# Performance work log

Hardware: AMD Instinct MI355X
Metric: run time of the kernel (lower is better)

## Reference

```python
import jax, jax.numpy as jnp
import numpy as np

H = 256
L = 5
B = 1024
NL, EL = 65536, 262144
NP_, EP = 131072, 524288
BN_EPS = 1e-5


def _bn_relu(x, gamma, beta):
    # BatchNorm1d (training mode, biased variance) followed by ReLU
    m = x.mean(axis=0)
    v = ((x - m) ** 2).mean(axis=0)
    return jax.nn.relu((x - m) * jax.lax.rsqrt(v + BN_EPS) * gamma + beta)


def _gin_conv(h, src, dst, W1, b1, W2, b2):
    # GINConv, eps=0: mlp(x + sum_{j->i} x_j)
    agg = jax.ops.segment_sum(h[src], dst, num_segments=h.shape[0])
    z = h + agg
    return jax.nn.relu(z @ W1 + b1) @ W2 + b2


def _forward(lig_x, prot_x, lig_embed_W, lig_embed_b, prot_embed_W, prot_embed_b,
             lig_virtual0, prot_virtual0,
             lig_conv_W1, lig_conv_b1, lig_conv_W2, lig_conv_b2,
             lig_vmlp_W, lig_vmlp_b, lig_vmlp_gamma, lig_vmlp_beta,
             prot_conv_W1, prot_conv_b1, prot_conv_W2, prot_conv_b2,
             prot_vmlp_W, prot_vmlp_b, prot_vmlp_gamma, prot_vmlp_beta,
             pred_W1, pred_b1, pred_W2, pred_b2,
             lig_batch, prot_batch, lig_edge_index, prot_edge_index):
    lig_h = lig_x @ lig_embed_W + lig_embed_b        # [NL, H]
    prot_h = prot_x @ prot_embed_W + prot_embed_b    # [NP, H]
    lig_v = jnp.broadcast_to(lig_virtual0, (B, H))
    prot_v = jnp.broadcast_to(prot_virtual0, (B, H))
    l_src, l_dst = lig_edge_index[0], lig_edge_index[1]
    p_src, p_dst = prot_edge_index[0], prot_edge_index[1]
    for i in range(L):
        # ligand branch: virtual-node pool -> MLP -> broadcast, then GIN conv (residual)
        lig_v = lig_v + jax.ops.segment_sum(lig_h, lig_batch, num_segments=B)
        lig_v = _bn_relu(lig_v @ lig_vmlp_W[i] + lig_vmlp_b[i], lig_vmlp_gamma[i], lig_vmlp_beta[i])
        lig_h = lig_h + lig_v[lig_batch]
        lig_h = lig_h + _gin_conv(lig_h, l_src, l_dst, lig_conv_W1[i], lig_conv_b1[i], lig_conv_W2[i], lig_conv_b2[i])
        # protein branch
        prot_v = prot_v + jax.ops.segment_sum(prot_h, prot_batch, num_segments=B)
        prot_v = _bn_relu(prot_v @ prot_vmlp_W[i] + prot_vmlp_b[i], prot_vmlp_gamma[i], prot_vmlp_beta[i])
        prot_h = prot_h + prot_v[prot_batch]
        prot_h = prot_h + _gin_conv(prot_h, p_src, p_dst, prot_conv_W1[i], prot_conv_b1[i], prot_conv_W2[i], prot_conv_b2[i])
    lig_cnt = jax.ops.segment_sum(jnp.ones((lig_h.shape[0],), lig_h.dtype), lig_batch, num_segments=B)
    prot_cnt = jax.ops.segment_sum(jnp.ones((prot_h.shape[0],), prot_h.dtype), prot_batch, num_segments=B)
    lig_pool = jax.ops.segment_sum(lig_h, lig_batch, num_segments=B) / lig_cnt[:, None]
    prot_pool = jax.ops.segment_sum(prot_h, prot_batch, num_segments=B) / prot_cnt[:, None]
    combined = jnp.concatenate([lig_pool, prot_pool], axis=-1)  # [B, 2H]
    return jax.nn.relu(combined @ pred_W1 + pred_b1) @ pred_W2 + pred_b2  # [B, 1]


def setup_inputs() -> dict:
    key = jax.random.key(0)
    ks = jax.random.split(key, 40)
    s = 0.05
    inp = {
        'lig_x': jax.random.normal(ks[0], (NL, 26), jnp.float32),
        'prot_x': jax.random.normal(ks[1], (NP_, 20), jnp.float32),
        'lig_embed_W': jax.random.normal(ks[2], (26, H), jnp.float32) * s,
        'lig_embed_b': jnp.zeros((H,), jnp.float32),
        'prot_embed_W': jax.random.normal(ks[3], (20, H), jnp.float32) * s,
        'prot_embed_b': jnp.zeros((H,), jnp.float32),
        'lig_virtual0': jax.random.normal(ks[4], (1, H), jnp.float32),
        'prot_virtual0': jax.random.normal(ks[5], (1, H), jnp.float32),
        'lig_conv_W1': jax.random.normal(ks[6], (L, H, H), jnp.float32) * s,
        'lig_conv_b1': jnp.zeros((L, H), jnp.float32),
        'lig_conv_W2': jax.random.normal(ks[7], (L, H, H), jnp.float32) * s,
        'lig_conv_b2': jnp.zeros((L, H), jnp.float32),
        'lig_vmlp_W': jax.random.normal(ks[8], (L, H, H), jnp.float32) * s,
        'lig_vmlp_b': jnp.zeros((L, H), jnp.float32),
        'lig_vmlp_gamma': jnp.ones((L, H), jnp.float32),
        'lig_vmlp_beta': jnp.zeros((L, H), jnp.float32),
        'prot_conv_W1': jax.random.normal(ks[9], (L, H, H), jnp.float32) * s,
        'prot_conv_b1': jnp.zeros((L, H), jnp.float32),
        'prot_conv_W2': jax.random.normal(ks[10], (L, H, H), jnp.float32) * s,
        'prot_conv_b2': jnp.zeros((L, H), jnp.float32),
        'prot_vmlp_W': jax.random.normal(ks[11], (L, H, H), jnp.float32) * s,
        'prot_vmlp_b': jnp.zeros((L, H), jnp.float32),
        'prot_vmlp_gamma': jnp.ones((L, H), jnp.float32),
        'prot_vmlp_beta': jnp.zeros((L, H), jnp.float32),
        'pred_W1': jax.random.normal(ks[12], (2 * H, H), jnp.float32) * s,
        'pred_b1': jnp.zeros((H,), jnp.float32),
        'pred_W2': jax.random.normal(ks[13], (H, 1), jnp.float32) * s,
        'pred_b2': jnp.zeros((1,), jnp.float32),
        # sorted batch ids covering all B graphs (PyG-style contiguous batching)
        'lig_batch': (jnp.arange(NL, dtype=jnp.int32) * B) // NL,
        'prot_batch': (jnp.arange(NP_, dtype=jnp.int32) * B) // NP_,
        'lig_edge_index': jax.random.randint(ks[14], (2, EL), 0, NL, jnp.int32),
        'prot_edge_index': jax.random.randint(ks[15], (2, EP), 0, NP_, jnp.int32),
    }
    return inp


def reference(lig_x, prot_x, lig_embed_W, lig_embed_b, prot_embed_W, prot_embed_b,
              lig_virtual0, prot_virtual0,
              lig_conv_W1, lig_conv_b1, lig_conv_W2, lig_conv_b2,
              lig_vmlp_W, lig_vmlp_b, lig_vmlp_gamma, lig_vmlp_beta,
              prot_conv_W1, prot_conv_b1, prot_conv_W2, prot_conv_b2,
              prot_vmlp_W, prot_vmlp_b, prot_vmlp_gamma, prot_vmlp_beta,
              pred_W1, pred_b1, pred_W2, pred_b2,
              lig_batch, prot_batch, lig_edge_index, prot_edge_index):
    return _forward(lig_x, prot_x, lig_embed_W, lig_embed_b, prot_embed_W, prot_embed_b,
                    lig_virtual0, prot_virtual0,
                    lig_conv_W1, lig_conv_b1, lig_conv_W2, lig_conv_b2,
                    lig_vmlp_W, lig_vmlp_b, lig_vmlp_gamma, lig_vmlp_beta,
                    prot_conv_W1, prot_conv_b1, prot_conv_W2, prot_conv_b2,
                    prot_vmlp_W, prot_vmlp_b, prot_vmlp_gamma, prot_vmlp_beta,
                    pred_W1, pred_b1, pred_W2, pred_b2,
                    lig_batch, prot_batch, lig_edge_index, prot_edge_index)
```

## Files before the change

kernel.cpp:

```cpp
#include <hip/hip_runtime.h>

#define H_DIM 256
#define NLAYER 5
#define BGRAPH 1024
#define CAP 16
#define OVF_CAP 4096

typedef __attribute__((ext_vector_type(8))) short short8;
typedef __attribute__((ext_vector_type(4))) float f32x4;
typedef const __attribute__((address_space(1))) unsigned int* gas_ptr;
typedef __attribute__((address_space(3))) unsigned int* las_ptr;

struct __align__(8) us4 { unsigned short x, y, z, w; };

__device__ __forceinline__ float b2f(unsigned short u) {
    union { float f; unsigned v; } c; c.v = ((unsigned)u) << 16; return c.f;
}
__device__ __forceinline__ unsigned short f2b(float f) {
    union { float f; unsigned v; } c; c.f = f;
    return (unsigned short)((c.v + 0x7fffu + ((c.v >> 16) & 1u)) >> 16);
}

__global__ __launch_bounds__(256) void embed_kernel(
    const float* __restrict__ x, const float* __restrict__ W,
    const float* __restrict__ b, unsigned short* __restrict__ h, int K)
{
    __shared__ float xs[256];
    const int m0 = blockIdx.x * 8;
    const int tid = threadIdx.x;
    if (tid < 8 * K) xs[tid] = x[(size_t)m0 * K + tid];
    __syncthreads();
    const int n = tid;
    float acc[8] = {0.f,0.f,0.f,0.f,0.f,0.f,0.f,0.f};
    for (int k = 0; k < K; ++k) {
        const float w = W[k * H_DIM + n];
        #pragma unroll
        for (int r = 0; r < 8; ++r) acc[r] += xs[r * K + k] * w;
    }
    const float bb = b[n];
    #pragma unroll
    for (int r = 0; r < 8; ++r)
        h[(size_t)(m0 + r) * H_DIM + n] = f2b(acc[r] + bb);
}

__global__ __launch_bounds__(256) void init_v_kernel(
    const float* __restrict__ lig0, const float* __restrict__ prot0,
    float* __restrict__ lig_v, float* __restrict__ prot_v)
{
    const int b = blockIdx.x, n = threadIdx.x;
    lig_v[b * H_DIM + n]  = lig0[n];
    prot_v[b * H_DIM + n] = prot0[n];
}

__global__ __launch_bounds__(256) void wprep_kernel(
    const float* __restrict__ W, unsigned short* __restrict__ Wt)
{
    __shared__ float t[64][65];
    const int l = blockIdx.z;
    const int k0 = blockIdx.x * 64, n0 = blockIdx.y * 64;
    const int tid = threadIdx.x;
    const int c = tid & 63, r4 = tid >> 6;
    const float* Wl = W + (size_t)l * 65536;
    unsigned short* Wtl = Wt + (size_t)l * 65536;
    #pragma unroll
    for (int i = 0; i < 16; ++i) {
        const int r = i * 4 + r4;
        t[r][c] = Wl[(size_t)(k0 + r) * 256 + n0 + c];
    }
    __syncthreads();
    #pragma unroll
    for (int i = 0; i < 16; ++i) {
        const int n = i * 4 + r4;
        Wtl[(size_t)(n0 + n) * 256 + k0 + c] = f2b(t[c][n]);
    }
}

__global__ __launch_bounds__(256) void bucket_build_kernel(
    const int* __restrict__ src, const int* __restrict__ dst, int E,
    int* __restrict__ deg, int* __restrict__ bucket,
    int* __restrict__ ovf, int* __restrict__ ovf_cnt)
{
    const int e = blockIdx.x * 256 + threadIdx.x;
    if (e >= E) return;
    const int d = dst[e], s = src[e];
    const int slot = atomicAdd(&deg[d], 1);
    if (slot < CAP) {
        bucket[(size_t)d * CAP + slot] = s;
    } else {
        const int o = atomicAdd(ovf_cnt, 1);
        if (o < OVF_CAP) { ovf[o * 2] = s; ovf[o * 2 + 1] = d; }
    }
}

__global__ __launch_bounds__(256) void pool_add_kernel(
    const unsigned short* __restrict__ h, float* __restrict__ v, int cnt)
{
    const int b = blockIdx.x, n = threadIdx.x;
    const unsigned short* hp = &h[(size_t)b * cnt * H_DIM + n];
    float s = 0.f;
    #pragma unroll 8
    for (int r = 0; r < cnt; ++r) s += b2f(hp[(size_t)r * H_DIM]);
    v[b * H_DIM + n] += s;
}

template<bool RELU>
__global__ __launch_bounds__(256) void gemm_small_kernel(
    const float* __restrict__ A, const float* __restrict__ W,
    const float* __restrict__ bias, float* __restrict__ C,
    int M, int N, int K)
{
    constexpr int BM = 32, BN = 64, BK = 32, TM = 2;
    __shared__ __align__(16) float As[BK][BM + 4];
    __shared__ __align__(16) float Bs[BK][BN];
    const int tid = threadIdx.x;
    const int tx = tid & 15;
    const int ty = tid >> 4;
    const int m0 = blockIdx.x * BM;
    const int n0 = blockIdx.y * BN;

    float acc[TM][4] = {};

    for (int kt = 0; kt < K; kt += BK) {
        {
            const int row = tid >> 3, kq = tid & 7;
            const float4 a = *(const float4*)&A[(size_t)(m0 + row) * K + kt + kq * 4];
            As[kq * 4 + 0][row] = a.x;
            As[kq * 4 + 1][row] = a.y;
            As[kq * 4 + 2][row] = a.z;
            As[kq * 4 + 3][row] = a.w;
        }
        #pragma unroll
        for (int i = 0; i < 2; ++i) {
            const int f = tid + i * 256;
            const int row = f >> 4, c4 = f & 15;
            *(float4*)&Bs[row][c4 * 4] =
                *(const float4*)&W[(size_t)(kt + row) * N + n0 + c4 * 4];
        }
        __syncthreads();
        #pragma unroll
        for (int kk = 0; kk < BK; ++kk) {
            const float4 bv = *(const float4*)&Bs[kk][tx * 4];
            #pragma unroll
            for (int im = 0; im < TM; ++im) {
                const float a = As[kk][ty * TM + im];
                acc[im][0] += a * bv.x; acc[im][1] += a * bv.y;
                acc[im][2] += a * bv.z; acc[im][3] += a * bv.w;
            }
        }
        __syncthreads();
    }

    const float4 bb = *(const float4*)&bias[n0 + tx * 4];
    #pragma unroll
    for (int im = 0; im < TM; ++im) {
        const int m = m0 + ty * TM + im;
        float4 r;
        r.x = acc[im][0] + bb.x; r.y = acc[im][1] + bb.y;
        r.z = acc[im][2] + bb.z; r.w = acc[im][3] + bb.w;
        if constexpr (RELU) {
            r.x = fmaxf(r.x, 0.f); r.y = fmaxf(r.y, 0.f);
            r.z = fmaxf(r.z, 0.f); r.w = fmaxf(r.w, 0.f);
        }
        *(float4*)&C[(size_t)m * N + n0 + tx * 4] = r;
    }
}

template<bool GEMM1>
__global__ __launch_bounds__(512) void conv_mfma_kernel(
    unsigned short* __restrict__ A, const unsigned short* __restrict__ Bt,
    const float* __restrict__ bias, unsigned short* __restrict__ Out)
{
    constexpr int K = 256, BM = 128, BK = 32;
    __shared__ unsigned short As[BM][BK];
    __shared__ unsigned short Bs[H_DIM][BK];
    const int tid  = threadIdx.x;
    const int lane = tid & 63;
    const int wid  = tid >> 6;
    const int wr   = wid >> 2;
    const int wc   = wid & 3;
    const int m0   = blockIdx.x * BM;

    f32x4 acc[4][4];
    #pragma unroll
    for (int i = 0; i < 4; ++i)
        #pragma unroll
        for (int j = 0; j < 4; ++j) acc[i][j] = (f32x4){0.f, 0.f, 0.f, 0.f};

    const int arow = tid >> 2, akq = tid & 3;
    const unsigned short* asrc0 = &A[(size_t)(m0 + arow) * K + akq * 8];
    const int albase = (tid & ~63) * 16;
    unsigned short* lAs = &As[0][0];
    unsigned short* lBs = &Bs[0][0];

    for (int kt = 0; kt < K; kt += BK) {
        __builtin_amdgcn_global_load_lds(
            (gas_ptr)(asrc0 + kt), (las_ptr)((char*)lAs + albase), 16, 0, 0);
        #pragma unroll
        for (int i = 0; i < 2; ++i) {
            const int c = tid + i * 512;
            const int n = c >> 2, kq = c & 3;
            __builtin_amdgcn_global_load_lds(
                (gas_ptr)&Bt[(size_t)n * K + kt + kq * 8],
                (las_ptr)((char*)lBs + albase + i * 512 * 16), 16, 0, 0);
        }
        __syncthreads();

        short8 av[4], bv[4];
        #pragma unroll
        for (int mi = 0; mi < 4; ++mi)
            av[mi] = *(const short8*)&As[wr * 64 + mi * 16 + (lane & 15)][(lane >> 4) * 8];
        #pragma unroll
        for (int ni = 0; ni < 4; ++ni)
            bv[ni] = *(const short8*)&Bs[wc * 64 + ni * 16 + (lane & 15)][(lane >> 4) * 8];
        #pragma unroll
        for (int mi = 0; mi < 4; ++mi)
            #pragma unroll
            for (int ni = 0; ni < 4; ++ni)
                acc[mi][ni] = __builtin_amdgcn_mfma_f32_16x16x32_bf16(
                    av[mi], bv[ni], acc[mi][ni], 0, 0, 0);
        __syncthreads();
    }

    #pragma unroll
    for (int ni = 0; ni < 4; ++ni) {
        const int col = wc * 64 + ni * 16 + (lane & 15);
        const float bb = bias[col];
        #pragma unroll
        for (int mi = 0; mi < 4; ++mi) {
            #pragma unroll
            for (int j = 0; j < 4; ++j) {
                const int row = m0 + wr * 64 + mi * 16 + ((lane >> 4) << 2) + j;
                const float val = acc[mi][ni][j] + bb;
                if constexpr (GEMM1) {
                    A[(size_t)row * H_DIM + col] = f2b(fmaxf(val, 0.f));
                } else {
                    unsigned short* op = &Out[(size_t)row * H_DIM + col];
                    *op = f2b(b2f(*op) + val);
                }
            }
        }
    }
}

__global__ __launch_bounds__(1024) void bn_stats_kernel(
    const float* __restrict__ vtmp, const float* __restrict__ gamma,
    const float* __restrict__ beta, float* __restrict__ scale,
    float* __restrict__ shift)
{
    __shared__ float ssum[4][256];
    __shared__ float ssq[4][256];
    const int n = threadIdx.x & 255;
    const int g = threadIdx.x >> 8;
    float s = 0.f, s2 = 0.f;
    #pragma unroll 8
    for (int r = g; r < BGRAPH; r += 4) {
        const float x = vtmp[(size_t)r * H_DIM + n];
        s += x; s2 += x * x;
    }
    ssum[g][n] = s; ssq[g][n] = s2;
    __syncthreads();
    if (g == 0) {
        s  = ssum[0][n] + ssum[1][n] + ssum[2][n] + ssum[3][n];
        s2 = ssq[0][n]  + ssq[1][n]  + ssq[2][n]  + ssq[3][n];
        const float mean = s * (1.f / BGRAPH);
        const float var  = s2 * (1.f / BGRAPH) - mean * mean;
        const float inv  = rsqrtf(var + 1e-5f);
        const float sc   = gamma[n] * inv;
        scale[n] = sc;
        shift[n] = beta[n] - mean * sc;
    }
}

__global__ __launch_bounds__(256) void bn_relu_kernel(
    const float* __restrict__ vtmp, const float* __restrict__ scale,
    const float* __restrict__ shift, float* __restrict__ v)
{
    const int idx = blockIdx.x * 256 + threadIdx.x;
    const int n = idx & 255;
    v[idx] = fmaxf(vtmp[idx] * scale[n] + shift[n], 0.f);
}

__global__ __launch_bounds__(256) void h_update_kernel(
    unsigned short* __restrict__ h,
    const float* __restrict__ v, const int* __restrict__ batch)
{
    const size_t i4 = (size_t)blockIdx.x * 256 + threadIdx.x;
    const int m = (int)(i4 >> 6);
    const int b = batch[m];
    const us4 hv = ((const us4*)h)[i4];
    const float4 vv = ((const float4*)v)[(size_t)b * 64 + (i4 & 63)];
    us4 o;
    o.x = f2b(b2f(hv.x) + vv.x); o.y = f2b(b2f(hv.y) + vv.y);
    o.z = f2b(b2f(hv.z) + vv.z); o.w = f2b(b2f(hv.w) + vv.w);
    ((us4*)h)[i4] = o;
}

__global__ __launch_bounds__(256) void gather_kernel(
    const unsigned short* __restrict__ h, const int* __restrict__ deg,
    const int* __restrict__ bucket, unsigned short* __restrict__ z)
{
    const int m = blockIdx.x * 4 + (threadIdx.x >> 6);
    const int lane = threadIdx.x & 63;
    int cnt = deg[m]; if (cnt > CAP) cnt = CAP;
    const us4 hv = *(const us4*)&h[(size_t)m * H_DIM + lane * 4];
    float4 acc = { b2f(hv.x), b2f(hv.y), b2f(hv.z), b2f(hv.w) };
    const int* bp = &bucket[(size_t)m * CAP];
    for (int i = 0; i < cnt; ++i) {
        const int s = bp[i];
        const us4 sv = *(const us4*)&h[(size_t)s * H_DIM + lane * 4];
        acc.x += b2f(sv.x); acc.y += b2f(sv.y);
        acc.z += b2f(sv.z); acc.w += b2f(sv.w);
    }
    us4 o = { f2b(acc.x), f2b(acc.y), f2b(acc.z), f2b(acc.w) };
    *(us4*)&z[(size_t)m * H_DIM + lane * 4] = o;
}

__global__ __launch_bounds__(64) void overflow_kernel(
    const int* __restrict__ ovf, const int* __restrict__ ovf_cnt,
    const unsigned short* __restrict__ h, unsigned short* __restrict__ z)
{
    int n = *ovf_cnt; if (n > OVF_CAP) n = OVF_CAP;
    const int lane = threadIdx.x;
    for (int i = 0; i < n; ++i) {
        const int s = ovf[i * 2], d = ovf[i * 2 + 1];
        const us4 sv = *(const us4*)&h[(size_t)s * H_DIM + lane * 4];
        us4* zp = (us4*)&z[(size_t)d * H_DIM + lane * 4];
        us4 zv = *zp;
        zv.x = f2b(b2f(zv.x) + b2f(sv.x)); zv.y = f2b(b2f(zv.y) + b2f(sv.y));
        zv.z = f2b(b2f(zv.z) + b2f(sv.z)); zv.w = f2b(b2f(zv.w) + b2f(sv.w));
        *zp = zv;
        __builtin_amdgcn_s_waitcnt(0);
    }
}

__global__ __launch_bounds__(256) void pool_final_kernel(
    const unsigned short* __restrict__ lig_h,
    const unsigned short* __restrict__ prot_h, float* __restrict__ comb)
{
    const int b = blockIdx.x, n = threadIdx.x;
    float s = 0.f;
    #pragma unroll 8
    for (int r = 0; r < 64; ++r) s += b2f(lig_h[(size_t)(b * 64 + r) * H_DIM + n]);
    comb[(size_t)b * 512 + n] = s * (1.f / 64.f);
    float s2 = 0.f;
    #pragma unroll 8
    for (int r = 0; r < 128; ++r) s2 += b2f(prot_h[(size_t)(b * 128 + r) * H_DIM + n]);
    comb[(size_t)b * 512 + 256 + n] = s2 * (1.f / 128.f);
}

__global__ __launch_bounds__(256) void pred_final_kernel(
    const float* __restrict__ hidden, const float* __restrict__ W2,
    const float* __restrict__ b2, float* __restrict__ out)
{
    const int b = blockIdx.x, t = threadIdx.x;
    float p = hidden[(size_t)b * H_DIM + t] * W2[t];
    #pragma unroll
    for (int off = 32; off >= 1; off >>= 1) p += __shfl_down(p, off);
    __shared__ float red[4];
    if ((t & 63) == 0) red[t >> 6] = p;
    __syncthreads();
    if (t == 0) out[b] = red[0] + red[1] + red[2] + red[3] + b2[0];
}

extern "C" void kernel_launch(void* const* d_in, const int* in_sizes, int n_in,
                              void* d_out, int out_size, void* d_ws, size_t ws_size,
                              hipStream_t stream)
{
    const int NL = 65536, NP = 131072, EL = 262144, EP = 524288;
    const int B = BGRAPH, H = H_DIM;

    const float* lig_x        = (const float*)d_in[0];
    const float* prot_x       = (const float*)d_in[1];
    const float* lig_embed_W  = (const float*)d_in[2];
    const float* lig_embed_b  = (const float*)d_in[3];
    const float* prot_embed_W = (const float*)d_in[4];
    const float* prot_embed_b = (const float*)d_in[5];
    const float* lig_virtual0 = (const float*)d_in[6];
    const float* prot_virtual0= (const float*)d_in[7];
    const float* lig_conv_W1  = (const float*)d_in[8];
    const float* lig_conv_b1  = (const float*)d_in[9];
    const float* lig_conv_W2  = (const float*)d_in[10];
    const float* lig_conv_b2  = (const float*)d_in[11];
    const float* lig_vmlp_W   = (const float*)d_in[12];
    const float* lig_vmlp_b   = (const float*)d_in[13];
    const float* lig_vmlp_g   = (const float*)d_in[14];
    const float* lig_vmlp_be  = (const float*)d_in[15];
    const float* prot_conv_W1 = (const float*)d_in[16];
    const float* prot_conv_b1 = (const float*)d_in[17];
    const float* prot_conv_W2 = (const float*)d_in[18];
    const float* prot_conv_b2 = (const float*)d_in[19];
    const float* prot_vmlp_W  = (const float*)d_in[20];
    const float* prot_vmlp_b  = (const float*)d_in[21];
    const float* prot_vmlp_g  = (const float*)d_in[22];
    const float* prot_vmlp_be = (const float*)d_in[23];
    const float* pred_W1      = (const float*)d_in[24];
    const float* pred_b1      = (const float*)d_in[25];
    const float* pred_W2      = (const float*)d_in[26];
    const float* pred_b2      = (const float*)d_in[27];
    const int* lig_batch      = (const int*)d_in[28];
    const int* prot_batch     = (const int*)d_in[29];
    const int* lig_ei         = (const int*)d_in[30];
    const int* prot_ei        = (const int*)d_in[31];

    float* ws = (float*)d_ws;
    float* lig_v  = ws;
    float* prot_v = lig_v  + (size_t)B * H;
    float* vtmp   = prot_v + (size_t)B * H;
    float* scale  = vtmp   + (size_t)B * H;
    float* shift  = scale  + H;
    float* comb   = shift  + H;
    float* hidden = comb   + (size_t)B * 2 * H;
    unsigned short* zbuf   = (unsigned short*)(hidden + (size_t)B * H);
    unsigned short* lig_h  = zbuf  + (size_t)NP * H;
    unsigned short* prot_h = lig_h + (size_t)NL * H;
    unsigned short* wt_lw1 = prot_h + (size_t)NP * H;
    unsigned short* wt_lw2 = wt_lw1 + (size_t)NLAYER * H * H;
    unsigned short* wt_pw1 = wt_lw2 + (size_t)NLAYER * H * H;
    unsigned short* wt_pw2 = wt_pw1 + (size_t)NLAYER * H * H;
    int* deg_lig  = (int*)(wt_pw2 + (size_t)NLAYER * H * H);
    int* deg_prot = deg_lig  + NL;
    int* bkt_lig  = deg_prot + NP;
    int* bkt_prot = bkt_lig  + (size_t)NL * CAP;
    int* ovf_lig  = bkt_prot + (size_t)NP * CAP;
    int* ovf_prot = ovf_lig  + OVF_CAP * 2;
    int* ovf_cnts = ovf_prot + OVF_CAP * 2;

    hipMemsetAsync(deg_lig, 0, (size_t)(NL + NP) * sizeof(int), stream);
    hipMemsetAsync(ovf_cnts, 0, 2 * sizeof(int), stream);
    bucket_build_kernel<<<EL / 256, 256, 0, stream>>>(
        lig_ei, lig_ei + EL, EL, deg_lig, bkt_lig, ovf_lig, ovf_cnts);
    bucket_build_kernel<<<EP / 256, 256, 0, stream>>>(
        prot_ei, prot_ei + EP, EP, deg_prot, bkt_prot, ovf_prot, ovf_cnts + 1);
    wprep_kernel<<<dim3(4, 4, NLAYER), 256, 0, stream>>>(lig_conv_W1, wt_lw1);
    wprep_kernel<<<dim3(4, 4, NLAYER), 256, 0, stream>>>(lig_conv_W2, wt_lw2);
    wprep_kernel<<<dim3(4, 4, NLAYER), 256, 0, stream>>>(prot_conv_W1, wt_pw1);
    wprep_kernel<<<dim3(4, 4, NLAYER), 256, 0, stream>>>(prot_conv_W2, wt_pw2);

    embed_kernel<<<NL / 8, 256, 0, stream>>>(lig_x, lig_embed_W, lig_embed_b, lig_h, 26);
    embed_kernel<<<NP / 8, 256, 0, stream>>>(prot_x, prot_embed_W, prot_embed_b, prot_h, 20);
    init_v_kernel<<<B, 256, 0, stream>>>(lig_virtual0, prot_virtual0, lig_v, prot_v);

    auto layer = [&](unsigned short* h, int Nn, int cnt, float* v,
                     const float* vW, const float* vb, const float* vg, const float* vbe,
                     const unsigned short* Wt1, const float* b1,
                     const unsigned short* Wt2, const float* b2,
                     const int* batch, const int* deg, const int* bkt,
                     const int* ovf, const int* ovf_cnt) {
        pool_add_kernel<<<B, 256, 0, stream>>>(h, v, cnt);
        gemm_small_kernel<false><<<dim3(B / 32, 4), 256, 0, stream>>>(
            v, vW, vb, vtmp, B, H, H);
        bn_stats_kernel<<<1, 1024, 0, stream>>>(vtmp, vg, vbe, scale, shift);
        bn_relu_kernel<<<B, 256, 0, stream>>>(vtmp, scale, shift, v);
        h_update_kernel<<<Nn / 4, 256, 0, stream>>>(h, v, batch);
        gather_kernel<<<Nn / 4, 256, 0, stream>>>(h, deg, bkt, zbuf);
        overflow_kernel<<<1, 64, 0, stream>>>(ovf, ovf_cnt, h, zbuf);
        conv_mfma_kernel<true><<<Nn / 128, 512, 0, stream>>>(zbuf, Wt1, b1, nullptr);
        conv_mfma_kernel<false><<<Nn / 128, 512, 0, stream>>>(zbuf, Wt2, b2, h);
    };

    for (int i = 0; i < NLAYER; ++i) {
        const size_t wo = (size_t)i * H * H;
        const size_t bo = (size_t)i * H;
        layer(lig_h, NL, 64, lig_v,
              lig_vmlp_W + wo, lig_vmlp_b + bo, lig_vmlp_g + bo, lig_vmlp_be + bo,
              wt_lw1 + wo, lig_conv_b1 + bo, wt_lw2 + wo, lig_conv_b2 + bo,
              lig_batch, deg_lig, bkt_lig, ovf_lig, ovf_cnts);
        layer(prot_h, NP, 128, prot_v,
              prot_vmlp_W + wo, prot_vmlp_b + bo, prot_vmlp_g + bo, prot_vmlp_be + bo,
              wt_pw1 + wo, prot_conv_b1 + bo, wt_pw2 + wo, prot_conv_b2 + bo,
              prot_batch, deg_prot, bkt_prot, ovf_prot, ovf_cnts + 1);
    }

    pool_final_kernel<<<B, 256, 0, stream>>>(lig_h, prot_h, comb);
    gemm_small_kernel<true><<<dim3(B / 32, 4), 256, 0, stream>>>(
        comb, pred_W1, pred_b1, hidden, B, H, 2 * H);
    pred_final_kernel<<<B, 256, 0, stream>>>(hidden, pred_W2, pred_b2, (float*)d_out);
}
```

Baseline: 2.163 ms.

## Fuse GIN MLP GEMMs and virtual-node update into gather and conv kernels

Fuses both GIN MLP GEMMs into one kernel that keeps the ReLU hidden tile in LDS. This removes the intermediate write and read of the hidden activations and one kernel launch. The separate h_update pass is dropped: the gather adds the virtual-node vector for each node and neighbor on the fly, and the conv epilogue applies the residual including v. The BN stats reduction is split into a 32-block partial pass plus a finalize pass instead of a single block. In exchange, the gather does extra batch and v lookups per neighbor, the conv tile is smaller (64 rows), and LDS use per block is higher.

```diff
diff --git a/kernel.cpp b/kernel.cpp
--- a/kernel.cpp
+++ b/kernel.cpp
@@ -165,55 +165,53 @@
     }
 }
 
-template<bool GEMM1>
-__global__ __launch_bounds__(512) void conv_mfma_kernel(
-    unsigned short* __restrict__ A, const unsigned short* __restrict__ Bt,
-    const float* __restrict__ bias, unsigned short* __restrict__ Out)
-{
-    constexpr int K = 256, BM = 128, BK = 32;
-    __shared__ unsigned short As[BM][BK];
-    __shared__ unsigned short Bs[H_DIM][BK];
+__global__ __launch_bounds__(512) void conv_fused_kernel(
+    const unsigned short* __restrict__ Z,
+    const unsigned short* __restrict__ Bt1, const float* __restrict__ b1,
+    const unsigned short* __restrict__ Bt2, const float* __restrict__ b2,
+    unsigned short* __restrict__ H, const float* __restrict__ v,
+    const int* __restrict__ batch)
+{
+    constexpr int K = 256, BK = 32;
+    __shared__ unsigned short As[64 * 32];
+    __shared__ unsigned short Bs[256 * 32];
+    __shared__ unsigned short Ts[64][264];
     const int tid  = threadIdx.x;
     const int lane = tid & 63;
     const int wid  = tid >> 6;
     const int wr   = wid >> 2;
     const int wc   = wid & 3;
-    const int m0   = blockIdx.x * BM;
-
-    f32x4 acc[4][4];
-    #pragma unroll
-    for (int i = 0; i < 4; ++i)
+    const int m0   = blockIdx.x * 64;
+    const int albase = (tid & ~63) * 16;
+
+    f32x4 acc[2][4];
+    #pragma unroll
+    for (int i = 0; i < 2; ++i)
         #pragma unroll
         for (int j = 0; j < 4; ++j) acc[i][j] = (f32x4){0.f, 0.f, 0.f, 0.f};
 
-    const int arow = tid >> 2, akq = tid & 3;
-    const unsigned short* asrc0 = &A[(size_t)(m0 + arow) * K + akq * 8];
-    const int albase = (tid & ~63) * 16;
-    unsigned short* lAs = &As[0][0];
-    unsigned short* lBs = &Bs[0][0];
-
     for (int kt = 0; kt < K; kt += BK) {
-        __builtin_amdgcn_global_load_lds(
-            (gas_ptr)(asrc0 + kt), (las_ptr)((char*)lAs + albase), 16, 0, 0);
+        if (tid < 256)
+            __builtin_amdgcn_global_load_lds(
+                (gas_ptr)&Z[(size_t)(m0 + (tid >> 2)) * K + kt + (tid & 3) * 8],
+                (las_ptr)((char*)As + albase), 16, 0, 0);
         #pragma unroll
         for (int i = 0; i < 2; ++i) {
             const int c = tid + i * 512;
-            const int n = c >> 2, kq = c & 3;
             __builtin_amdgcn_global_load_lds(
-                (gas_ptr)&Bt[(size_t)n * K + kt + kq * 8],
-                (las_ptr)((char*)lBs + albase + i * 512 * 16), 16, 0, 0);
+                (gas_ptr)&Bt1[(size_t)(c >> 2) * K + kt + (c & 3) * 8],
+                (las_ptr)((char*)Bs + albase + i * 8192), 16, 0, 0);
         }
         __syncthreads();
-
-        short8 av[4], bv[4];
-        #pragma unroll
-        for (int mi = 0; mi < 4; ++mi)
-            av[mi] = *(const short8*)&As[wr * 64 + mi * 16 + (lane & 15)][(lane >> 4) * 8];
+        short8 av[2], bv[4];
+        #pragma unroll
+        for (int mi = 0; mi < 2; ++mi)
+            av[mi] = *(const short8*)&As[(wr * 32 + mi * 16 + (lane & 15)) * 32 + (lane >> 4) * 8];
         #pragma unroll
         for (int ni = 0; ni < 4; ++ni)
-            bv[ni] = *(const short8*)&Bs[wc * 64 + ni * 16 + (lane & 15)][(lane >> 4) * 8];
-        #pragma unroll
-        for (int mi = 0; mi < 4; ++mi)
+            bv[ni] = *(const short8*)&Bs[(wc * 64 + ni * 16 + (lane & 15)) * 32 + (lane >> 4) * 8];
+        #pragma unroll
+        for (int mi = 0; mi < 2; ++mi)
             #pragma unroll
             for (int ni = 0; ni < 4; ++ni)
                 acc[mi][ni] = __builtin_amdgcn_mfma_f32_16x16x32_bf16(
@@ -224,51 +222,94 @@
     #pragma unroll
     for (int ni = 0; ni < 4; ++ni) {
         const int col = wc * 64 + ni * 16 + (lane & 15);
-        const float bb = bias[col];
-        #pragma unroll
-        for (int mi = 0; mi < 4; ++mi) {
+        const float bb = b1[col];
+        #pragma unroll
+        for (int mi = 0; mi < 2; ++mi)
             #pragma unroll
             for (int j = 0; j < 4; ++j) {
-                const int row = m0 + wr * 64 + mi * 16 + ((lane >> 4) << 2) + j;
-                const float val = acc[mi][ni][j] + bb;
-                if constexpr (GEMM1) {
-                    A[(size_t)row * H_DIM + col] = f2b(fmaxf(val, 0.f));
-                } else {
-                    unsigned short* op = &Out[(size_t)row * H_DIM + col];
-                    *op = f2b(b2f(*op) + val);
-                }
+                const int row = wr * 32 + mi * 16 + ((lane >> 4) << 2) + j;
+                Ts[row][col] = f2b(fmaxf(acc[mi][ni][j] + bb, 0.f));
             }
-        }
-    }
-}
-
-__global__ __launch_bounds__(1024) void bn_stats_kernel(
-    const float* __restrict__ vtmp, const float* __restrict__ gamma,
+    }
+    #pragma unroll
+    for (int i = 0; i < 2; ++i)
+        #pragma unroll
+        for (int j = 0; j < 4; ++j) acc[i][j] = (f32x4){0.f, 0.f, 0.f, 0.f};
+    __syncthreads();
+
+    for (int kt = 0; kt < K; kt += BK) {
+        #pragma unroll
+        for (int i = 0; i < 2; ++i) {
+            const int c = tid + i * 512;
+            __builtin_amdgcn_global_load_lds(
+                (gas_ptr)&Bt2[(size_t)(c >> 2) * K + kt + (c & 3) * 8],
+                (las_ptr)((char*)Bs + albase + i * 8192), 16, 0, 0);
+        }
+        __syncthreads();
+        short8 av[2], bv[4];
+        #pragma unroll
+        for (int mi = 0; mi < 2; ++mi)
+            av[mi] = *(const short8*)&Ts[wr * 32 + mi * 16 + (lane & 15)][kt + (lane >> 4) * 8];
+        #pragma unroll
+        for (int ni = 0; ni < 4; ++ni)
+            bv[ni] = *(const short8*)&Bs[(wc * 64 + ni * 16 + (lane & 15)) * 32 + (lane >> 4) * 8];
+        #pragma unroll
+        for (int mi = 0; mi < 2; ++mi)
+            #pragma unroll
+            for (int ni = 0; ni < 4; ++ni)
+                acc[mi][ni] = __builtin_amdgcn_mfma_f32_16x16x32_bf16(
+                    av[mi], bv[ni], acc[mi][ni], 0, 0, 0);
+        __syncthreads();
+    }
+
+    #pragma unroll
+    for (int mi = 0; mi < 2; ++mi)
+        #pragma unroll
+        for (int j = 0; j < 4; ++j) {
+            const int row = m0 + wr * 32 + mi * 16 + ((lane >> 4) << 2) + j;
+            const int bq = batch[row];
+            const float* vrow = &v[(size_t)bq * H_DIM];
+            #pragma unroll
+            for (int ni = 0; ni < 4; ++ni) {
+                const int col = wc * 64 + ni * 16 + (lane & 15);
+                unsigned short* hp = &H[(size_t)row * H_DIM + col];
+                const float hup = b2f(*hp) + vrow[col];
+                *hp = f2b(hup + acc[mi][ni][j] + b2[col]);
+            }
+        }
+}
+
+__global__ __launch_bounds__(256) void bn_part_kernel(
+    const float* __restrict__ vtmp, float* __restrict__ part)
+{
+    const int g = blockIdx.x, n = threadIdx.x;
+    float s = 0.f, s2 = 0.f;
+    #pragma unroll 8
+    for (int r = 0; r < 32; ++r) {
+        const float x = vtmp[(size_t)(g * 32 + r) * H_DIM + n];
+        s += x; s2 += x * x;
+    }
+    part[g * H_DIM + n] = s;
+    part[32 * H_DIM + g * H_DIM + n] = s2;
+}
+
+__global__ __launch_bounds__(256) void bn_finalize_kernel(
+    const float* __restrict__ part, const float* __restrict__ gamma,
     const float* __restrict__ beta, float* __restrict__ scale,
     float* __restrict__ shift)
 {
-    __shared__ float ssum[4][256];
-    __shared__ float ssq[4][256];
-    const int n = threadIdx.x & 255;
-    const int g = threadIdx.x >> 8;
+    const int n = threadIdx.x;
     float s = 0.f, s2 = 0.f;
     #pragma unroll 8
-    for (int r = g; r < BGRAPH; r += 4) {
-        const float x = vtmp[(size_t)r * H_DIM + n];
-        s += x; s2 += x * x;
-    }
-    ssum[g][n] = s; ssq[g][n] = s2;
-    __syncthreads();
-    if (g == 0) {
-        s  = ssum[0][n] + ssum[1][n] + ssum[2][n] + ssum[3][n];
-        s2 = ssq[0][n]  + ssq[1][n]  + ssq[2][n]  + ssq[3][n];
-        const float mean = s * (1.f / BGRAPH);
-        const float var  = s2 * (1.f / BGRAPH) - mean * mean;
-        const float inv  = rsqrtf(var + 1e-5f);
-        const float sc   = gamma[n] * inv;
-        scale[n] = sc;
-        shift[n] = beta[n] - mean * sc;
-    }
+    for (int g = 0; g < 32; ++g) {
+        s  += part[g * H_DIM + n];
+        s2 += part[32 * H_DIM + g * H_DIM + n];
+    }
+    const float mean = s * (1.f / BGRAPH);
+    const float var  = s2 * (1.f / BGRAPH) - mean * mean;
+    const float sc   = gamma[n] * rsqrtf(var + 1e-5f);
+    scale[n] = sc;
+    shift[n] = beta[n] - mean * sc;
 }
 
 __global__ __launch_bounds__(256) void bn_relu_kernel(
@@ -280,36 +321,50 @@
     v[idx] = fmaxf(vtmp[idx] * scale[n] + shift[n], 0.f);
 }
 
-__global__ __launch_bounds__(256) void h_update_kernel(
-    unsigned short* __restrict__ h,
-    const float* __restrict__ v, const int* __restrict__ batch)
-{
-    const size_t i4 = (size_t)blockIdx.x * 256 + threadIdx.x;
-    const int m = (int)(i4 >> 6);
-    const int b = batch[m];
-    const us4 hv = ((const us4*)h)[i4];
-    const float4 vv = ((const float4*)v)[(size_t)b * 64 + (i4 & 63)];
-    us4 o;
-    o.x = f2b(b2f(hv.x) + vv.x); o.y = f2b(b2f(hv.y) + vv.y);
-    o.z = f2b(b2f(hv.z) + vv.z); o.w = f2b(b2f(hv.w) + vv.w);
-    ((us4*)h)[i4] = o;
-}
-
-__global__ __launch_bounds__(256) void gather_kernel(
-    const unsigned short* __restrict__ h, const int* __restrict__ deg,
+__global__ __launch_bounds__(256) void gather2_kernel(
+    const unsigned short* __restrict__ h, const float* __restrict__ v,
+    const int* __restrict__ batch, const int* __restrict__ deg,
     const int* __restrict__ bucket, unsigned short* __restrict__ z)
 {
     const int m = blockIdx.x * 4 + (threadIdx.x >> 6);
     const int lane = threadIdx.x & 63;
     int cnt = deg[m]; if (cnt > CAP) cnt = CAP;
     const us4 hv = *(const us4*)&h[(size_t)m * H_DIM + lane * 4];
-    float4 acc = { b2f(hv.x), b2f(hv.y), b2f(hv.z), b2f(hv.w) };
+    const int bm = batch[m];
+    const float4 vm = *(const float4*)&v[(size_t)bm * H_DIM + lane * 4];
+    float4 acc = { b2f(hv.x) + vm.x, b2f(hv.y) + vm.y,
+                   b2f(hv.z) + vm.z, b2f(hv.w) + vm.w };
     const int* bp = &bucket[(size_t)m * CAP];
-    for (int i = 0; i < cnt; ++i) {
-        const int s = bp[i];
-        const us4 sv = *(const us4*)&h[(size_t)s * H_DIM + lane * 4];
-        acc.x += b2f(sv.x); acc.y += b2f(sv.y);
-        acc.z += b2f(sv.z); acc.w += b2f(sv.w);
+    for (int i = 0; i < cnt; i += 4) {
+        const int4 s4 = *(const int4*)&bp[i];
+        const int rem = cnt - i;
+        us4 a0, a1, a2, a3;
+        int q0, q1, q2, q3;
+        a0 = *(const us4*)&h[(size_t)s4.x * H_DIM + lane * 4];
+        q0 = batch[s4.x];
+        if (rem > 1) { a1 = *(const us4*)&h[(size_t)s4.y * H_DIM + lane * 4]; q1 = batch[s4.y]; }
+        if (rem > 2) { a2 = *(const us4*)&h[(size_t)s4.z * H_DIM + lane * 4]; q2 = batch[s4.z]; }
+        if (rem > 3) { a3 = *(const us4*)&h[(size_t)s4.w * H_DIM + lane * 4]; q3 = batch[s4.w]; }
+        {
+            const float4 w0 = *(const float4*)&v[(size_t)q0 * H_DIM + lane * 4];
+            acc.x += b2f(a0.x) + w0.x; acc.y += b2f(a0.y) + w0.y;
+            acc.z += b2f(a0.z) + w0.z; acc.w += b2f(a0.w) + w0.w;
+        }
+        if (rem > 1) {
+            const float4 w1 = *(const float4*)&v[(size_t)q1 * H_DIM + lane * 4];
+            acc.x += b2f(a1.x) + w1.x; acc.y += b2f(a1.y) + w1.y;
+            acc.z += b2f(a1.z) + w1.z; acc.w += b2f(a1.w) + w1.w;
+        }
+        if (rem > 2) {
+            const float4 w2 = *(const float4*)&v[(size_t)q2 * H_DIM + lane * 4];
+            acc.x += b2f(a2.x) + w2.x; acc.y += b2f(a2.y) + w2.y;
+            acc.z += b2f(a2.z) + w2.z; acc.w += b2f(a2.w) + w2.w;
+        }
+        if (rem > 3) {
+            const float4 w3 = *(const float4*)&v[(size_t)q3 * H_DIM + lane * 4];
+            acc.x += b2f(a3.x) + w3.x; acc.y += b2f(a3.y) + w3.y;
+            acc.z += b2f(a3.z) + w3.z; acc.w += b2f(a3.w) + w3.w;
+        }
     }
     us4 o = { f2b(acc.x), f2b(acc.y), f2b(acc.z), f2b(acc.w) };
     *(us4*)&z[(size_t)m * H_DIM + lane * 4] = o;
@@ -317,17 +372,22 @@
 
 __global__ __launch_bounds__(64) void overflow_kernel(
     const int* __restrict__ ovf, const int* __restrict__ ovf_cnt,
-    const unsigned short* __restrict__ h, unsigned short* __restrict__ z)
+    const unsigned short* __restrict__ h, const float* __restrict__ v,
+    const int* __restrict__ batch, unsigned short* __restrict__ z)
 {
     int n = *ovf_cnt; if (n > OVF_CAP) n = OVF_CAP;
     const int lane = threadIdx.x;
     for (int i = 0; i < n; ++i) {
         const int s = ovf[i * 2], d = ovf[i * 2 + 1];
+        const int bs = batch[s];
         const us4 sv = *(const us4*)&h[(size_t)s * H_DIM + lane * 4];
+        const float4 vs = *(const float4*)&v[(size_t)bs * H_DIM + lane * 4];
         us4* zp = (us4*)&z[(size_t)d * H_DIM + lane * 4];
         us4 zv = *zp;
-        zv.x = f2b(b2f(zv.x) + b2f(sv.x)); zv.y = f2b(b2f(zv.y) + b2f(sv.y));
-        zv.z = f2b(b2f(zv.z) + b2f(sv.z)); zv.w = f2b(b2f(zv.w) + b2f(sv.w));
+        zv.x = f2b(b2f(zv.x) + b2f(sv.x) + vs.x);
+        zv.y = f2b(b2f(zv.y) + b2f(sv.y) + vs.y);
+        zv.z = f2b(b2f(zv.z) + b2f(sv.z) + vs.z);
+        zv.w = f2b(b2f(zv.w) + b2f(sv.w) + vs.w);
         *zp = zv;
         __builtin_amdgcn_s_waitcnt(0);
     }
@@ -408,7 +468,8 @@
     float* vtmp   = prot_v + (size_t)B * H;
     float* scale  = vtmp   + (size_t)B * H;
     float* shift  = scale  + H;
-    float* comb   = shift  + H;
+    float* part   = shift  + H;
+    float* comb   = part   + 64 * H;
     float* hidden = comb   + (size_t)B * 2 * H;
     unsigned short* zbuf   = (unsigned short*)(hidden + (size_t)B * H);
     unsigned short* lig_h  = zbuf  + (size_t)NP * H;
@@ -449,13 +510,13 @@
         pool_add_kernel<<<B, 256, 0, stream>>>(h, v, cnt);
         gemm_small_kernel<false><<<dim3(B / 32, 4), 256, 0, stream>>>(
             v, vW, vb, vtmp, B, H, H);
-        bn_stats_kernel<<<1, 1024, 0, stream>>>(vtmp, vg, vbe, scale, shift);
+        bn_part_kernel<<<32, 256, 0, stream>>>(vtmp, part);
+        bn_finalize_kernel<<<1, 256, 0, stream>>>(part, vg, vbe, scale, shift);
         bn_relu_kernel<<<B, 256, 0, stream>>>(vtmp, scale, shift, v);
-        h_update_kernel<<<Nn / 4, 256, 0, stream>>>(h, v, batch);
-        gather_kernel<<<Nn / 4, 256, 0, stream>>>(h, deg, bkt, zbuf);
-        overflow_kernel<<<1, 64, 0, stream>>>(ovf, ovf_cnt, h, zbuf);
-        conv_mfma_kernel<true><<<Nn / 128, 512, 0, stream>>>(zbuf, Wt1, b1, nullptr);
-        conv_mfma_kernel<false><<<Nn / 128, 512, 0, stream>>>(zbuf, Wt2, b2, h);
+        gather2_kernel<<<Nn / 4, 256, 0, stream>>>(h, v, batch, deg, bkt, zbuf);
+        overflow_kernel<<<1, 64, 0, stream>>>(ovf, ovf_cnt, h, v, batch, zbuf);
+        conv_fused_kernel<<<Nn / 64, 512, 0, stream>>>(
+            zbuf, Wt1, b1, Wt2, b2, h, v, batch);
     };
 
     for (int i = 0; i < NLAYER; ++i) {
```

Result: faster. 1.799 ms (-16.8%).
